# Kernel optimization log

Measured on AMD Instinct MI355X. Metric: run time of the kernel, lower is better.

The kernel has to match this reference:

```python
import jax, jax.numpy as jnp
import numpy as np

B, S, D_MODEL = 2, 4096, 2048
N_IDX_HEADS, D_HEAD = 4, 64


def setup_inputs() -> dict:
    key = jax.random.key(0)
    k1, k2, k3 = jax.random.split(key, 3)
    h = jax.random.normal(k1, (B, S, D_MODEL), dtype=jnp.float32)
    # torch Linear weights: [out_features, in_features]
    Wq = jax.random.normal(k2, (N_IDX_HEADS * D_HEAD, D_MODEL), dtype=jnp.float32) * (D_MODEL ** -0.5)
    Wk = jax.random.normal(k3, (D_HEAD, D_MODEL), dtype=jnp.float32) * (D_MODEL ** -0.5)
    w = jnp.ones((N_IDX_HEADS,), dtype=jnp.float32)
    return {"h": h, "Wq": Wq, "Wk": Wk, "w": w}


def reference(h, Wq, Wk, w):
    batch, seq, _ = h.shape
    # q: [B, T, H, Dh]; k: [B, S, Dh]
    q = (h @ Wq.T).reshape(batch, seq, N_IDX_HEADS, D_HEAD)
    k = h @ Wk.T
    # scores: [B, T, H, S]
    scores = jax.nn.relu(jnp.einsum('bthd,bsd->bths', q, k))
    # head-weighted sum -> I: [B, T, S]
    I = jnp.einsum('bths,h->bts', scores, w)
    return I
```

## Files before the change

### kernel.cpp

```cpp
#include <hip/hip_runtime.h>

typedef __attribute__((ext_vector_type(8))) short bf16x8;
typedef __attribute__((ext_vector_type(4))) float f32x4;
typedef __attribute__((ext_vector_type(8))) unsigned short us8;

#define K_DIM 2048
#define QK_N  320
#define SEQ   4096
#define BK    64
#define NCHUNK (K_DIM / BK)
#define CHUNK_BYTES (QK_N * BK * 2)

__device__ __forceinline__ unsigned short f2bf(float f) {
    unsigned int u = __builtin_bit_cast(unsigned int, f);
    u += 0x7FFFu + ((u >> 16) & 1u);
    return (unsigned short)(u >> 16);
}

__device__ __forceinline__ void gld_lds16(const void* g, void* l) {
    __builtin_amdgcn_global_load_lds(
        (const __attribute__((address_space(1))) void*)g,
        (__attribute__((address_space(3))) void*)l,
        16, 0, 0);
}

__global__ void cvt_w_swz(const float* __restrict__ Wq,
                          const float* __restrict__ Wk,
                          unsigned short* __restrict__ ws) {
    int id = blockIdx.x * 256 + threadIdx.x;
    int c  = id >> 8;
    int k8 = id & 255;
    int k0 = k8 * 8;
    const float* src = (c < 256) ? (Wq + (size_t)c * K_DIM + k0)
                                 : (Wk + (size_t)(c - 256) * K_DIM + k0);
    float4 v0 = *reinterpret_cast<const float4*>(src);
    float4 v1 = *reinterpret_cast<const float4*>(src + 4);
    us8 o;
    o[0] = f2bf(v0.x); o[1] = f2bf(v0.y); o[2] = f2bf(v0.z); o[3] = f2bf(v0.w);
    o[4] = f2bf(v1.x); o[5] = f2bf(v1.y); o[6] = f2bf(v1.z); o[7] = f2bf(v1.w);
    int kc = k0 / BK;
    int u  = (k0 % BK) >> 3;
    size_t byteoff = (size_t)kc * CHUNK_BYTES + ((size_t)(u * QK_N + c) * 16);
    *reinterpret_cast<us8*>((char*)ws + byteoff) = o;
}

__global__ __launch_bounds__(512, 2) void proj_gemm(
    const float* __restrict__ A,
    const unsigned short* __restrict__ Wsz,
    unsigned short* __restrict__ C)
{
    __shared__ unsigned short Bs[2][CHUNK_BYTES / 2];

    const int tid  = threadIdx.x;
    const int lane = tid & 63;
    const int wid  = tid >> 6;
    const int rg   = wid >> 2;
    const int cg   = wid & 3;
    const int row0 = blockIdx.x * 32 + rg * 16;
    const int col0 = cg * 80;
    const int lr   = lane & 15;
    const int lg   = lane >> 4;

    const float* ap = A + (size_t)(row0 + lr) * K_DIM + lg * 8;

    f32x4 acc[5];
#pragma unroll
    for (int j = 0; j < 5; ++j) acc[j] = (f32x4)0.f;

    const char* wsrc = (const char*)Wsz;
    auto stage = [&](int kc, int buf) {
        const char* src = wsrc + (size_t)kc * CHUNK_BYTES + wid * 5120 + lane * 16;
        char* dst = (char*)&Bs[buf][0] + wid * 5120 + lane * 16;
#pragma unroll
        for (int i = 0; i < 5; ++i)
            gld_lds16(src + i * 1024, dst + i * 1024);
    };

    auto loadA = [&](int kc, float4& f0, float4& f1, float4& f2, float4& f3) {
        const float* p = ap + (size_t)kc * BK;
        f0 = *reinterpret_cast<const float4*>(p);
        f1 = *reinterpret_cast<const float4*>(p + 4);
        f2 = *reinterpret_cast<const float4*>(p + 32);
        f3 = *reinterpret_cast<const float4*>(p + 36);
    };

    auto compute = [&](int buf, float4 f0, float4 f1, float4 f2, float4 f3) {
        const char* base = (const char*)&Bs[buf][0];
#pragma unroll
        for (int ks = 0; ks < 2; ++ks) {
            bf16x8 a;
            float4 x = ks ? f2 : f0, y = ks ? f3 : f1;
            a[0] = (short)f2bf(x.x); a[1] = (short)f2bf(x.y);
            a[2] = (short)f2bf(x.z); a[3] = (short)f2bf(x.w);
            a[4] = (short)f2bf(y.x); a[5] = (short)f2bf(y.y);
            a[6] = (short)f2bf(y.z); a[7] = (short)f2bf(y.w);
            const char* ub = base + (size_t)(ks * 4 + lg) * (QK_N * 16);
#pragma unroll
            for (int j = 0; j < 5; ++j) {
                int c = col0 + j * 16 + lr;
                bf16x8 b = *reinterpret_cast<const bf16x8*>(ub + (size_t)c * 16);
                acc[j] = __builtin_amdgcn_mfma_f32_16x16x32_bf16(a, b, acc[j], 0, 0, 0);
            }
        }
    };

#define WAIT_BAR() do { \
        asm volatile("s_waitcnt vmcnt(4) lgkmcnt(0)" ::: "memory"); \
        __builtin_amdgcn_s_barrier(); \
    } while (0)

    float4 a0, a1, a2, a3, b0, b1, b2, b3;
    stage(0, 0);
    loadA(0, a0, a1, a2, a3);
    WAIT_BAR();

    for (int kc = 0; kc < NCHUNK; kc += 2) {
        stage(kc + 1, 1);
        loadA(kc + 1, b0, b1, b2, b3);
        compute(0, a0, a1, a2, a3);
        WAIT_BAR();
        if (kc + 2 < NCHUNK) {
            stage(kc + 2, 0);
            loadA(kc + 2, a0, a1, a2, a3);
        }
        compute(1, b0, b1, b2, b3);
        WAIT_BAR();
    }
#undef WAIT_BAR

#pragma unroll
    for (int j = 0; j < 5; ++j)
#pragma unroll
        for (int r = 0; r < 4; ++r)
            C[(size_t)(row0 + lg * 4 + r) * QK_N + col0 + j * 16 + lr] =
                f2bf(acc[j][r]);
}

__global__ __launch_bounds__(256) void scores_kernel(
    const unsigned short* __restrict__ QK,
    const float* __restrict__ w,
    float* __restrict__ out)
{
    const int lane = threadIdx.x & 63;
    const int wid  = threadIdx.x >> 6;
    const int b  = blockIdx.z;
    const int t0 = blockIdx.y * 128 + (wid >> 1) * 64;
    const int s0 = blockIdx.x * 128 + (wid & 1) * 64;

    const int lr = lane & 15;
    const int lk = (lane >> 4) * 8;

    const unsigned short* Qb = QK + (size_t)b * SEQ * QK_N;
    const unsigned short* Kb = Qb + 256;

    float wv[4] = { w[0], w[1], w[2], w[3] };

    f32x4 fin[4][4];
#pragma unroll
    for (int i = 0; i < 4; ++i)
#pragma unroll
        for (int j = 0; j < 4; ++j) fin[i][j] = (f32x4)0.f;

    const unsigned short* qp = Qb + (size_t)(t0 + lr) * QK_N + lk;
    const unsigned short* kp = Kb + (size_t)(s0 + lr) * QK_N + lk;

#pragma unroll
    for (int h = 0; h < 4; ++h) {
        f32x4 acc[4][4];
#pragma unroll
        for (int i = 0; i < 4; ++i)
#pragma unroll
            for (int j = 0; j < 4; ++j) acc[i][j] = (f32x4)0.f;

#pragma unroll
        for (int ks = 0; ks < 2; ++ks) {
            bf16x8 a[4], bb[4];
#pragma unroll
            for (int i = 0; i < 4; ++i)
                a[i] = *reinterpret_cast<const bf16x8*>(
                    qp + (size_t)i * 16 * QK_N + h * 64 + ks * 32);
#pragma unroll
            for (int j = 0; j < 4; ++j)
                bb[j] = *reinterpret_cast<const bf16x8*>(
                    kp + (size_t)j * 16 * QK_N + ks * 32);
#pragma unroll
            for (int i = 0; i < 4; ++i)
#pragma unroll
                for (int j = 0; j < 4; ++j)
                    acc[i][j] = __builtin_amdgcn_mfma_f32_16x16x32_bf16(a[i], bb[j], acc[i][j], 0, 0, 0);
        }
#pragma unroll
        for (int i = 0; i < 4; ++i)
#pragma unroll
            for (int j = 0; j < 4; ++j)
#pragma unroll
                for (int r = 0; r < 4; ++r)
                    fin[i][j][r] += wv[h] * fmaxf(acc[i][j][r], 0.f);
    }

    const int orow = (lane >> 4) * 4;
    float* ob = out + (size_t)b * SEQ * SEQ;
#pragma unroll
    for (int i = 0; i < 4; ++i)
#pragma unroll
        for (int j = 0; j < 4; ++j)
#pragma unroll
            for (int r = 0; r < 4; ++r)
                ob[(size_t)(t0 + i * 16 + orow + r) * SEQ + s0 + j * 16 + lr] =
                    fin[i][j][r];
}

extern "C" void kernel_launch(void* const* d_in, const int* in_sizes, int n_in,
                              void* d_out, int out_size, void* d_ws, size_t ws_size,
                              hipStream_t stream) {
    const float* h  = (const float*)d_in[0];
    const float* Wq = (const float*)d_in[1];
    const float* Wk = (const float*)d_in[2];
    const float* w  = (const float*)d_in[3];
    float* out = (float*)d_out;

    unsigned short* W_swz = (unsigned short*)d_ws;
    unsigned short* QKb   = (unsigned short*)((char*)d_ws + (size_t)NCHUNK * CHUNK_BYTES);

    cvt_w_swz<<<320, 256, 0, stream>>>(Wq, Wk, W_swz);
    proj_gemm<<<256, 512, 0, stream>>>(h, W_swz, QKb);
    scores_kernel<<<dim3(32, 32, 2), 256, 0, stream>>>(QKb, w, out);
}
```

Measured before the change: 113.3 us.

## Retile projection GEMM with LDS-staged A and vectorize score stores

The projection GEMM is retiled to 64-row by 160-column blocks: the weight matrix is split into two column halves, and the fp32 activation tile is converted to bf16 once and staged through LDS, where all warps share it. Before, each wave converted its own A fragment in registers. The intent is to cut redundant A loads and conversions and to reshape the grid. In the scores kernel the MFMA operands are swapped so each lane holds four consecutive output columns, which allows float4 stores instead of scattered scalar stores. The cost is more LDS traffic, a more complex pipeline with its own wait counts, and some extra weight reloads across the two column halves.

```diff
diff --git a/kernel.cpp b/kernel.cpp
--- a/kernel.cpp
+++ b/kernel.cpp
@@ -8,8 +8,10 @@
 #define QK_N  320
 #define SEQ   4096
 #define BK    64
-#define NCHUNK (K_DIM / BK)
-#define CHUNK_BYTES (QK_N * BK * 2)
+#define NCHUNK 32
+#define NHALF  160
+#define BM     64
+#define BCHUNK 20480
 
 __device__ __forceinline__ unsigned short f2bf(float f) {
     unsigned int u = __builtin_bit_cast(unsigned int, f);
@@ -38,9 +40,12 @@
     us8 o;
     o[0] = f2bf(v0.x); o[1] = f2bf(v0.y); o[2] = f2bf(v0.z); o[3] = f2bf(v0.w);
     o[4] = f2bf(v1.x); o[5] = f2bf(v1.y); o[6] = f2bf(v1.z); o[7] = f2bf(v1.w);
+    int half = (c >= NHALF) ? 1 : 0;
+    int cc   = c - half * NHALF;
     int kc = k0 / BK;
     int u  = (k0 % BK) >> 3;
-    size_t byteoff = (size_t)kc * CHUNK_BYTES + ((size_t)(u * QK_N + c) * 16);
+    size_t byteoff = (size_t)half * (NCHUNK * (size_t)BCHUNK)
+                   + (size_t)kc * BCHUNK + ((size_t)(u * NHALF + cc) * 16);
     *reinterpret_cast<us8*>((char*)ws + byteoff) = o;
 }
 
@@ -49,91 +54,112 @@
     const unsigned short* __restrict__ Wsz,
     unsigned short* __restrict__ C)
 {
-    __shared__ unsigned short Bs[2][CHUNK_BYTES / 2];
+    __shared__ unsigned short Asm[2][BM * BK];
+    __shared__ unsigned short Bsm[2][BCHUNK / 2];
 
     const int tid  = threadIdx.x;
     const int lane = tid & 63;
     const int wid  = tid >> 6;
-    const int rg   = wid >> 2;
-    const int cg   = wid & 3;
-    const int row0 = blockIdx.x * 32 + rg * 16;
-    const int col0 = cg * 80;
-    const int lr   = lane & 15;
-    const int lg   = lane >> 4;
-
-    const float* ap = A + (size_t)(row0 + lr) * K_DIM + lg * 8;
+    const int rg   = wid >> 1;
+    const int cg   = wid & 1;
+    const int mrow0 = blockIdx.y * BM;
+    const int half  = blockIdx.x;
+    const int lr = lane & 15, lg = lane >> 4;
+
+    const int ar = tid >> 3;
+    const int au = tid & 7;
+    const float* a_src = A + (size_t)(mrow0 + ar) * K_DIM + au * 8;
+    const int a_dst_off = ((au << 6) + ar) << 4;
+
+    const char* wsrc = (const char*)Wsz + (size_t)half * (NCHUNK * (size_t)BCHUNK)
+                     + wid * 1024 + lane * 16;
 
     f32x4 acc[5];
 #pragma unroll
     for (int j = 0; j < 5; ++j) acc[j] = (f32x4)0.f;
 
-    const char* wsrc = (const char*)Wsz;
-    auto stage = [&](int kc, int buf) {
-        const char* src = wsrc + (size_t)kc * CHUNK_BYTES + wid * 5120 + lane * 16;
-        char* dst = (char*)&Bs[buf][0] + wid * 5120 + lane * 16;
-#pragma unroll
-        for (int i = 0; i < 5; ++i)
-            gld_lds16(src + i * 1024, dst + i * 1024);
-    };
-
-    auto loadA = [&](int kc, float4& f0, float4& f1, float4& f2, float4& f3) {
-        const float* p = ap + (size_t)kc * BK;
+    auto stageB = [&](int kc, int buf) {
+        const char* s = wsrc + (size_t)kc * BCHUNK;
+        char* d = (char*)&Bsm[buf][0] + wid * 1024 + lane * 16;
+        gld_lds16(s, d);
+        gld_lds16(s + 8192, d + 8192);
+        if (wid < 4) gld_lds16(s + 16384, d + 16384);
+    };
+    auto loadA = [&](int kc, float4& f0, float4& f1) {
+        const float* p = a_src + (size_t)kc * BK;
         f0 = *reinterpret_cast<const float4*>(p);
         f1 = *reinterpret_cast<const float4*>(p + 4);
-        f2 = *reinterpret_cast<const float4*>(p + 32);
-        f3 = *reinterpret_cast<const float4*>(p + 36);
-    };
-
-    auto compute = [&](int buf, float4 f0, float4 f1, float4 f2, float4 f3) {
-        const char* base = (const char*)&Bs[buf][0];
+    };
+    auto writeA = [&](float4 f0, float4 f1, int buf) {
+        us8 o;
+        o[0] = f2bf(f0.x); o[1] = f2bf(f0.y); o[2] = f2bf(f0.z); o[3] = f2bf(f0.w);
+        o[4] = f2bf(f1.x); o[5] = f2bf(f1.y); o[6] = f2bf(f1.z); o[7] = f2bf(f1.w);
+        *reinterpret_cast<us8*>((char*)&Asm[buf][0] + a_dst_off) = o;
+    };
+    auto compute = [&](int buf) {
+        const char* ab = (const char*)&Asm[buf][0];
+        const char* bb = (const char*)&Bsm[buf][0];
 #pragma unroll
         for (int ks = 0; ks < 2; ++ks) {
-            bf16x8 a;
-            float4 x = ks ? f2 : f0, y = ks ? f3 : f1;
-            a[0] = (short)f2bf(x.x); a[1] = (short)f2bf(x.y);
-            a[2] = (short)f2bf(x.z); a[3] = (short)f2bf(x.w);
-            a[4] = (short)f2bf(y.x); a[5] = (short)f2bf(y.y);
-            a[6] = (short)f2bf(y.z); a[7] = (short)f2bf(y.w);
-            const char* ub = base + (size_t)(ks * 4 + lg) * (QK_N * 16);
+            const int u = ks * 4 + lg;
+            bf16x8 a = *reinterpret_cast<const bf16x8*>(
+                ab + (((u << 6) + rg * 16 + lr) << 4));
+            const char* bu = bb + (size_t)u * (NHALF * 16);
 #pragma unroll
             for (int j = 0; j < 5; ++j) {
-                int c = col0 + j * 16 + lr;
-                bf16x8 b = *reinterpret_cast<const bf16x8*>(ub + (size_t)c * 16);
+                bf16x8 b = *reinterpret_cast<const bf16x8*>(
+                    bu + ((cg * 80 + j * 16 + lr) << 4));
                 acc[j] = __builtin_amdgcn_mfma_f32_16x16x32_bf16(a, b, acc[j], 0, 0, 0);
             }
         }
     };
 
-#define WAIT_BAR() do { \
-        asm volatile("s_waitcnt vmcnt(4) lgkmcnt(0)" ::: "memory"); \
+#define WAIT_BAR(N) do { \
+        asm volatile("s_waitcnt vmcnt(" #N ") lgkmcnt(0)" ::: "memory"); \
         __builtin_amdgcn_s_barrier(); \
     } while (0)
 
-    float4 a0, a1, a2, a3, b0, b1, b2, b3;
-    stage(0, 0);
-    loadA(0, a0, a1, a2, a3);
-    WAIT_BAR();
-
-    for (int kc = 0; kc < NCHUNK; kc += 2) {
-        stage(kc + 1, 1);
-        loadA(kc + 1, b0, b1, b2, b3);
-        compute(0, a0, a1, a2, a3);
-        WAIT_BAR();
-        if (kc + 2 < NCHUNK) {
-            stage(kc + 2, 0);
-            loadA(kc + 2, a0, a1, a2, a3);
-        }
-        compute(1, b0, b1, b2, b3);
-        WAIT_BAR();
+    float4 r0a, r0b;
+    float4 r1a, r1b;
+
+    stageB(0, 0);
+    loadA(0, r0a, r0b);
+    asm volatile("s_waitcnt vmcnt(0)" ::: "memory");
+    writeA(r0a, r0b, 0);
+    loadA(1, r1a, r1b);
+    asm volatile("s_waitcnt lgkmcnt(0)" ::: "memory");
+    __builtin_amdgcn_s_barrier();
+
+    for (int t = 0; t < NCHUNK; t += 2) {
+        stageB(t + 1, 1);
+        {
+            int kc = (t + 2 < NCHUNK) ? t + 2 : NCHUNK - 1;
+            loadA(kc, r0a, r0b);
+        }
+        compute(0);
+        writeA(r1a, r1b, 1);
+        WAIT_BAR(2);
+        const int u = t + 1;
+        if (u < NCHUNK - 1) {
+            stageB(u + 1, 0);
+            int kc = (u + 2 < NCHUNK) ? u + 2 : NCHUNK - 1;
+            loadA(kc, r1a, r1b);
+        }
+        compute(1);
+        if (u < NCHUNK - 1) {
+            writeA(r0a, r0b, 0);
+            WAIT_BAR(2);
+        }
     }
 #undef WAIT_BAR
 
+    const int crow = mrow0 + rg * 16 + lg * 4;
+    const int ccol = half * NHALF + cg * 80 + lr;
 #pragma unroll
     for (int j = 0; j < 5; ++j)
 #pragma unroll
         for (int r = 0; r < 4; ++r)
-            C[(size_t)(row0 + lg * 4 + r) * QK_N + col0 + j * 16 + lr] =
-                f2bf(acc[j][r]);
+            C[(size_t)(crow + r) * QK_N + ccol + j * 16] = f2bf(acc[j][r]);
 }
 
 __global__ __launch_bounds__(256) void scores_kernel(
@@ -149,6 +175,7 @@
 
     const int lr = lane & 15;
     const int lk = (lane >> 4) * 8;
+    const int lg = lane >> 4;
 
     const unsigned short* Qb = QK + (size_t)b * SEQ * QK_N;
     const unsigned short* Kb = Qb + 256;
@@ -174,20 +201,20 @@
 
 #pragma unroll
         for (int ks = 0; ks < 2; ++ks) {
-            bf16x8 a[4], bb[4];
+            bf16x8 qf[4], kf[4];
 #pragma unroll
             for (int i = 0; i < 4; ++i)
-                a[i] = *reinterpret_cast<const bf16x8*>(
+                qf[i] = *reinterpret_cast<const bf16x8*>(
                     qp + (size_t)i * 16 * QK_N + h * 64 + ks * 32);
 #pragma unroll
             for (int j = 0; j < 4; ++j)
-                bb[j] = *reinterpret_cast<const bf16x8*>(
+                kf[j] = *reinterpret_cast<const bf16x8*>(
                     kp + (size_t)j * 16 * QK_N + ks * 32);
 #pragma unroll
             for (int i = 0; i < 4; ++i)
 #pragma unroll
                 for (int j = 0; j < 4; ++j)
-                    acc[i][j] = __builtin_amdgcn_mfma_f32_16x16x32_bf16(a[i], bb[j], acc[i][j], 0, 0, 0);
+                    acc[i][j] = __builtin_amdgcn_mfma_f32_16x16x32_bf16(kf[j], qf[i], acc[i][j], 0, 0, 0);
         }
 #pragma unroll
         for (int i = 0; i < 4; ++i)
@@ -198,16 +225,18 @@
                     fin[i][j][r] += wv[h] * fmaxf(acc[i][j][r], 0.f);
     }
 
-    const int orow = (lane >> 4) * 4;
     float* ob = out + (size_t)b * SEQ * SEQ;
 #pragma unroll
-    for (int i = 0; i < 4; ++i)
-#pragma unroll
-        for (int j = 0; j < 4; ++j)
-#pragma unroll
-            for (int r = 0; r < 4; ++r)
-                ob[(size_t)(t0 + i * 16 + orow + r) * SEQ + s0 + j * 16 + lr] =
-                    fin[i][j][r];
+    for (int i = 0; i < 4; ++i) {
+        const size_t rbase = (size_t)(t0 + i * 16 + lr) * SEQ + s0 + lg * 4;
+#pragma unroll
+        for (int j = 0; j < 4; ++j) {
+            float4 v;
+            v.x = fin[i][j][0]; v.y = fin[i][j][1];
+            v.z = fin[i][j][2]; v.w = fin[i][j][3];
+            *reinterpret_cast<float4*>(&ob[rbase + j * 16]) = v;
+        }
+    }
 }
 
 extern "C" void kernel_launch(void* const* d_in, const int* in_sizes, int n_in,
@@ -220,9 +249,9 @@
     float* out = (float*)d_out;
 
     unsigned short* W_swz = (unsigned short*)d_ws;
-    unsigned short* QKb   = (unsigned short*)((char*)d_ws + (size_t)NCHUNK * CHUNK_BYTES);
+    unsigned short* QKb   = (unsigned short*)((char*)d_ws + 2 * (size_t)NCHUNK * BCHUNK);
 
     cvt_w_swz<<<320, 256, 0, stream>>>(Wq, Wk, W_swz);
-    proj_gemm<<<256, 512, 0, stream>>>(h, W_swz, QKb);
+    proj_gemm<<<dim3(2, 128), 512, 0, stream>>>(h, W_swz, QKb);
     scores_kernel<<<dim3(32, 32, 2), 256, 0, stream>>>(QKb, w, out);
 }
```

New measurement: 111.6 us. Within noise of the previous version (-1.4%).
